# Optimization experiments

Measured on AMD Instinct MI355X. Metric: run time of the kernel, lower is better.

## Reference

```python
import jax, jax.numpy as jnp
import numpy as np

EPS = 1e-4  # matches init_kwargs eps


def setup_inputs() -> dict:
    key = jax.random.key(0)
    k1, k2, k3 = jax.random.split(key, 3)
    B, C, T = 64, 256, 2048
    x = jax.random.normal(k1, (B, C, T), dtype=jnp.float32)
    # per-timestep BatchNorm affine params: [T, C]
    gamma = 1.0 + 0.1 * jax.random.normal(k2, (T, C), dtype=jnp.float32)
    beta = 0.01 * jax.random.normal(k3, (T, C), dtype=jnp.float32)
    return {"x": x, "gamma": gamma, "beta": beta}


def reference(x, gamma, beta):
    # BNTTv1 (training mode): every timestep's BatchNorm1d sees the FULL [B, C, T]
    # tensor, so the batch statistics (per-channel mean/var over B and T) are
    # identical across timesteps. Only the affine (gamma_t, beta_t) differs, and
    # the module keeps just slice t of layer t's output. Equivalent fused form:
    mean = jnp.mean(x, axis=(0, 2), keepdims=True)            # [1, C, 1]
    var = jnp.mean((x - mean) ** 2, axis=(0, 2), keepdims=True)  # biased var
    norm = (x - mean) * jax.lax.rsqrt(var + EPS)              # [B, C, T]
    # gamma/beta: [T, C] -> broadcast as [1, C, T]
    out = norm * gamma.T[None, :, :] + beta.T[None, :, :]
    return out
```

## Files before the change

### kernel.cpp

```cpp
#include <hip/hip_runtime.h>

#define B_ 64
#define C_ 256
#define T_ 2048
#define EPS_ 1e-4f
#define NPC ((float)(B_ * T_))

#define T4 (T_ / 4)
#define CG_ 8

#define CTILE 16
#define T4TILE 16
#define BCHUNK 32

typedef float f4 __attribute__((ext_vector_type(4)));

__global__ __launch_bounds__(256) void bntt_stats(const float* __restrict__ x,
                                                  float* __restrict__ partials) {
    const int bid = blockIdx.x;
    const int b   = bid >> 5;
    const int cg  = bid & 31;
    const int tid = threadIdx.x;
    const f4* p = (const f4*)(x + ((size_t)b * C_ + (size_t)cg * CG_) * T_);

    float sum[CG_], ssq[CG_];
    #pragma unroll
    for (int k = 0; k < CG_; ++k) { sum[k] = 0.0f; ssq[k] = 0.0f; }

    #pragma unroll
    for (int i = 0; i < 16; ++i) {
        f4 v = p[tid + i * 256];
        const int k = i >> 1;
        sum[k] += v.x + v.y + v.z + v.w;
        ssq[k] += v.x * v.x + v.y * v.y + v.z * v.z + v.w * v.w;
    }

    __shared__ float ls[CG_][256];
    __shared__ float lq[CG_][256];
    #pragma unroll
    for (int k = 0; k < CG_; ++k) { ls[k][tid] = sum[k]; lq[k][tid] = ssq[k]; }
    __syncthreads();

    const int k = tid >> 5;
    const int j = tid & 31;
    float S = 0.0f, SS = 0.0f;
    #pragma unroll
    for (int m = 0; m < 8; ++m) {
        S  += ls[k][j + m * 32];
        SS += lq[k][j + m * 32];
    }
    #pragma unroll
    for (int off = 16; off > 0; off >>= 1) {
        S  += __shfl_down(S, off);
        SS += __shfl_down(SS, off);
    }
    if (j == 0) {
        const size_t c = (size_t)cg * CG_ + k;
        partials[(size_t)b * C_ + c]                      = S;
        partials[(size_t)B_ * C_ + (size_t)b * C_ + c]    = SS;
    }
}

__global__ __launch_bounds__(256) void bntt_norm(const float* __restrict__ x,
                                                 const float* __restrict__ gamma,
                                                 const float* __restrict__ beta,
                                                 const float* __restrict__ partials,
                                                 float* __restrict__ out) {
    __shared__ float sg[64][17];
    __shared__ float sb[64][17];
    __shared__ float psum[CTILE][8], psq[CTILE][8];
    __shared__ float smean[CTILE], sistd[CTILE];

    const int tid    = threadIdx.x;
    const int tile   = blockIdx.x & 511;
    const int c0     = (tile >> 5) * CTILE;
    const int t4base = (tile & 31) * T4TILE;
    const int b0     = (blockIdx.x >> 9) * BCHUNK;

    {
        const int cl  = tid & 15;
        const int tl0 = tid >> 4;
        const int tbase = t4base * 4;
        #pragma unroll
        for (int it = 0; it < 4; ++it) {
            const int tl = tl0 + it * 16;
            const size_t gi = (size_t)(tbase + tl) * C_ + (c0 + cl);
            sg[tl][cl] = gamma[gi];
            sb[tl][cl] = beta[gi];
        }
    }

    if (tid < 128) {
        const int cl = tid & 15;
        const int h  = tid >> 4;
        const int c  = c0 + cl;
        float S = 0.0f, SS = 0.0f;
        #pragma unroll
        for (int m = 0; m < 8; ++m) {
            const size_t b = (size_t)(h * 8 + m);
            S  += partials[b * C_ + c];
            SS += partials[(size_t)B_ * C_ + b * C_ + c];
        }
        psum[cl][h] = S;
        psq[cl][h]  = SS;
    }
    __syncthreads();

    if (tid < CTILE) {
        float S = 0.0f, SS = 0.0f;
        #pragma unroll
        for (int h = 0; h < 8; ++h) { S += psum[tid][h]; SS += psq[tid][h]; }
        const float mean = S / NPC;
        smean[tid] = mean;
        sistd[tid] = rsqrtf(SS / NPC - mean * mean + EPS_);
    }
    __syncthreads();

    const int t4i = tid & 15;
    const int ci  = tid >> 4;
    const float mean = smean[ci];
    const float istd = sistd[ci];
    f4 sc, sh;
    #pragma unroll
    for (int j = 0; j < 4; ++j) {
        const int tl = t4i * 4 + j;
        const float s1 = sg[tl][ci] * istd;
        ((float*)&sc)[j] = s1;
        ((float*)&sh)[j] = fmaf(-mean, s1, sb[tl][ci]);
    }

    size_t idx = ((size_t)b0 * C_ + (c0 + ci)) * T4 + (t4base + t4i);
    const size_t step = (size_t)C_ * T4;
    #pragma unroll 8
    for (int b = 0; b < BCHUNK; ++b) {
        f4 xv = ((const f4*)x)[idx];
        f4 o;
        o.x = fmaf(xv.x, sc.x, sh.x);
        o.y = fmaf(xv.y, sc.y, sh.y);
        o.z = fmaf(xv.z, sc.z, sh.z);
        o.w = fmaf(xv.w, sc.w, sh.w);
        __builtin_nontemporal_store(o, &((f4*)out)[idx]);
        idx += step;
    }
}

#define SPLITS 8
#define BPB (B_ / SPLITS)
__global__ __launch_bounds__(256) void bntt_stats_fb(const float* __restrict__ x,
                                                     float* __restrict__ partials) {
    const int c   = blockIdx.x & (C_ - 1);
    const int s   = blockIdx.x >> 8;
    const int tid = threadIdx.x;
    float sum = 0.0f, sumsq = 0.0f;
    const int b0 = s * BPB;
    #pragma unroll
    for (int b = 0; b < BPB; ++b) {
        const f4* p = (const f4*)(x + (size_t)(b0 + b) * (C_ * T_) + (size_t)c * T_);
        #pragma unroll
        for (int i = 0; i < T4 / 256; ++i) {
            f4 v = p[tid + i * 256];
            sum   += v.x + v.y + v.z + v.w;
            sumsq += v.x * v.x + v.y * v.y + v.z * v.z + v.w * v.w;
        }
    }
    #pragma unroll
    for (int off = 32; off > 0; off >>= 1) {
        sum   += __shfl_down(sum, off);
        sumsq += __shfl_down(sumsq, off);
    }
    __shared__ float ls2[4], lss2[4];
    const int wave = tid >> 6, lane = tid & 63;
    if (lane == 0) { ls2[wave] = sum; lss2[wave] = sumsq; }
    __syncthreads();
    if (tid == 0) {
        partials[s * C_ + c]               = ls2[0] + ls2[1] + ls2[2] + ls2[3];
        partials[SPLITS * C_ + s * C_ + c] = lss2[0] + lss2[1] + lss2[2] + lss2[3];
    }
}

__global__ __launch_bounds__(256) void bntt_norm_fb(const float* __restrict__ x,
                                                    const float* __restrict__ gamma,
                                                    const float* __restrict__ beta,
                                                    const float* __restrict__ partials,
                                                    float* __restrict__ out) {
    const int p   = (blockIdx.x & 511) * 256 + threadIdx.x;
    const int c   = p >> 9;
    const int t4  = p & (T4 - 1);
    const int t   = t4 * 4;
    const int b0  = (blockIdx.x >> 9) * BCHUNK;

    float S = 0.0f, SS = 0.0f;
    #pragma unroll
    for (int s = 0; s < SPLITS; ++s) {
        S  += partials[s * C_ + c];
        SS += partials[SPLITS * C_ + s * C_ + c];
    }
    const float mean = S / NPC;
    const float istd = rsqrtf(SS / NPC - mean * mean + EPS_);

    f4 sc, sh;
    #pragma unroll
    for (int j = 0; j < 4; ++j) {
        float g  = gamma[(size_t)(t + j) * C_ + c];
        float bb = beta [(size_t)(t + j) * C_ + c];
        float s1 = g * istd;
        ((float*)&sc)[j] = s1;
        ((float*)&sh)[j] = fmaf(-mean, s1, bb);
    }
    size_t idx = (size_t)(b0 * C_ + c) * T4 + t4;
    const size_t step = (size_t)C_ * T4;
    #pragma unroll 8
    for (int b = 0; b < BCHUNK; ++b) {
        f4 xv = ((const f4*)x)[idx];
        f4 o;
        o.x = fmaf(xv.x, sc.x, sh.x);
        o.y = fmaf(xv.y, sc.y, sh.y);
        o.z = fmaf(xv.z, sc.z, sh.z);
        o.w = fmaf(xv.w, sc.w, sh.w);
        __builtin_nontemporal_store(o, &((f4*)out)[idx]);
        idx += step;
    }
}

extern "C" void kernel_launch(void* const* d_in, const int* in_sizes, int n_in,
                              void* d_out, int out_size, void* d_ws, size_t ws_size,
                              hipStream_t stream) {
    const float* x     = (const float*)d_in[0];
    const float* gamma = (const float*)d_in[1];
    const float* beta  = (const float*)d_in[2];
    float* out = (float*)d_out;
    float* partials = (float*)d_ws;

    const int ngrid = (C_ / CTILE) * (T4 / T4TILE) * (B_ / BCHUNK);

    if (ws_size >= (size_t)2 * B_ * C_ * sizeof(float)) {
        bntt_stats<<<B_ * (C_ / CG_), 256, 0, stream>>>(x, partials);
        bntt_norm<<<ngrid, 256, 0, stream>>>(x, gamma, beta, partials, out);
    } else {
        bntt_stats_fb<<<C_ * SPLITS, 256, 0, stream>>>(x, partials);
        bntt_norm_fb<<<ngrid, 256, 0, stream>>>(x, gamma, beta, partials, out);
    }
}
```

Baseline: 256.4 us.

## Fuse stats and normalize into one persistent kernel with global atomic barrier

```diff
diff --git a/kernel.cpp b/kernel.cpp
--- a/kernel.cpp
+++ b/kernel.cpp
@@ -9,74 +9,82 @@
 #define T4 (T_ / 4)
 #define CG_ 8
 
+#define NBLK 1024
 #define CTILE 16
 #define T4TILE 16
 #define BCHUNK 32
 
 typedef float f4 __attribute__((ext_vector_type(4)));
 
-__global__ __launch_bounds__(256) void bntt_stats(const float* __restrict__ x,
-                                                  float* __restrict__ partials) {
+__global__ __launch_bounds__(256, 6) void bntt_onepass(const float* __restrict__ x,
+                                                       const float* __restrict__ gamma,
+                                                       const float* __restrict__ beta,
+                                                       float* __restrict__ out,
+                                                       float* __restrict__ ws) {
+    float* partials   = ws;
+    unsigned int* bar = (unsigned int*)(ws + 2 * B_ * C_);
+
+    const int tid = threadIdx.x;
     const int bid = blockIdx.x;
-    const int b   = bid >> 5;
-    const int cg  = bid & 31;
-    const int tid = threadIdx.x;
-    const f4* p = (const f4*)(x + ((size_t)b * C_ + (size_t)cg * CG_) * T_);
-
-    float sum[CG_], ssq[CG_];
-    #pragma unroll
-    for (int k = 0; k < CG_; ++k) { sum[k] = 0.0f; ssq[k] = 0.0f; }
-
-    #pragma unroll
-    for (int i = 0; i < 16; ++i) {
-        f4 v = p[tid + i * 256];
-        const int k = i >> 1;
-        sum[k] += v.x + v.y + v.z + v.w;
-        ssq[k] += v.x * v.x + v.y * v.y + v.z * v.z + v.w * v.w;
-    }
 
     __shared__ float ls[CG_][256];
     __shared__ float lq[CG_][256];
-    #pragma unroll
-    for (int k = 0; k < CG_; ++k) { ls[k][tid] = sum[k]; lq[k][tid] = ssq[k]; }
-    __syncthreads();
-
-    const int k = tid >> 5;
-    const int j = tid & 31;
-    float S = 0.0f, SS = 0.0f;
-    #pragma unroll
-    for (int m = 0; m < 8; ++m) {
-        S  += ls[k][j + m * 32];
-        SS += lq[k][j + m * 32];
-    }
-    #pragma unroll
-    for (int off = 16; off > 0; off >>= 1) {
-        S  += __shfl_down(S, off);
-        SS += __shfl_down(SS, off);
-    }
-    if (j == 0) {
-        const size_t c = (size_t)cg * CG_ + k;
-        partials[(size_t)b * C_ + c]                      = S;
-        partials[(size_t)B_ * C_ + (size_t)b * C_ + c]    = SS;
-    }
-}
-
-__global__ __launch_bounds__(256) void bntt_norm(const float* __restrict__ x,
-                                                 const float* __restrict__ gamma,
-                                                 const float* __restrict__ beta,
-                                                 const float* __restrict__ partials,
-                                                 float* __restrict__ out) {
-    __shared__ float sg[64][17];
-    __shared__ float sb[64][17];
     __shared__ float psum[CTILE][8], psq[CTILE][8];
     __shared__ float smean[CTILE], sistd[CTILE];
 
-    const int tid    = threadIdx.x;
-    const int tile   = blockIdx.x & 511;
+    const int ab    = bid >> 4;
+    const int cpair = bid & 15;
+    #pragma unroll
+    for (int half = 0; half < 2; ++half) {
+        const int cbase = cpair * (2 * CG_) + half * CG_;
+        const f4* p = (const f4*)(x + ((size_t)ab * C_ + cbase) * T_);
+
+        float sum[CG_], ssq[CG_];
+        #pragma unroll
+        for (int k = 0; k < CG_; ++k) { sum[k] = 0.0f; ssq[k] = 0.0f; }
+        #pragma unroll
+        for (int i = 0; i < 16; ++i) {
+            f4 v = p[tid + i * 256];
+            const int k = i >> 1;
+            sum[k] += v.x + v.y + v.z + v.w;
+            ssq[k] += v.x * v.x + v.y * v.y + v.z * v.z + v.w * v.w;
+        }
+        #pragma unroll
+        for (int k = 0; k < CG_; ++k) { ls[k][tid] = sum[k]; lq[k][tid] = ssq[k]; }
+        __syncthreads();
+
+        const int k = tid >> 5;
+        const int j = tid & 31;
+        float S = 0.0f, SS = 0.0f;
+        #pragma unroll
+        for (int m = 0; m < 8; ++m) {
+            S  += ls[k][j + m * 32];
+            SS += lq[k][j + m * 32];
+        }
+        #pragma unroll
+        for (int off = 16; off > 0; off >>= 1) {
+            S  += __shfl_down(S, off);
+            SS += __shfl_down(SS, off);
+        }
+        if (j == 0) {
+            const size_t c = (size_t)cbase + k;
+            __hip_atomic_store(&partials[(size_t)ab * C_ + c], S,
+                               __ATOMIC_RELAXED, __HIP_MEMORY_SCOPE_AGENT);
+            __hip_atomic_store(&partials[(size_t)B_ * C_ + (size_t)ab * C_ + c], SS,
+                               __ATOMIC_RELAXED, __HIP_MEMORY_SCOPE_AGENT);
+        }
+        __syncthreads();
+    }
+    if (tid == 0)
+        __hip_atomic_fetch_add(bar, 1u, __ATOMIC_RELEASE, __HIP_MEMORY_SCOPE_AGENT);
+
+    const int tile   = bid & 511;
     const int c0     = (tile >> 5) * CTILE;
     const int t4base = (tile & 31) * T4TILE;
-    const int b0     = (blockIdx.x >> 9) * BCHUNK;
-
+    const int b0     = (bid >> 9) * BCHUNK;
+
+    float (*sg)[17] = (float (*)[17])ls;
+    float (*sb)[17] = (float (*)[17])lq;
     {
         const int cl  = tid & 15;
         const int tl0 = tid >> 4;
@@ -90,22 +98,30 @@
         }
     }
 
+    if (tid == 0) {
+        while (__hip_atomic_load(bar, __ATOMIC_ACQUIRE, __HIP_MEMORY_SCOPE_AGENT)
+               < (unsigned int)NBLK)
+            __builtin_amdgcn_s_sleep(2);
+    }
+    __syncthreads();
+
     if (tid < 128) {
         const int cl = tid & 15;
         const int h  = tid >> 4;
-        const int c  = c0 + cl;
+        const size_t c = (size_t)(c0 + cl);
         float S = 0.0f, SS = 0.0f;
         #pragma unroll
         for (int m = 0; m < 8; ++m) {
-            const size_t b = (size_t)(h * 8 + m);
-            S  += partials[b * C_ + c];
-            SS += partials[(size_t)B_ * C_ + b * C_ + c];
+            const size_t bb = (size_t)(h * 8 + m);
+            S  += __hip_atomic_load(&partials[bb * C_ + c],
+                                    __ATOMIC_RELAXED, __HIP_MEMORY_SCOPE_AGENT);
+            SS += __hip_atomic_load(&partials[(size_t)B_ * C_ + bb * C_ + c],
+                                    __ATOMIC_RELAXED, __HIP_MEMORY_SCOPE_AGENT);
         }
         psum[cl][h] = S;
         psq[cl][h]  = SS;
     }
     __syncthreads();
-
     if (tid < CTILE) {
         float S = 0.0f, SS = 0.0f;
         #pragma unroll
@@ -229,15 +245,16 @@
     const float* gamma = (const float*)d_in[1];
     const float* beta  = (const float*)d_in[2];
     float* out = (float*)d_out;
-    float* partials = (float*)d_ws;
-
-    const int ngrid = (C_ / CTILE) * (T4 / T4TILE) * (B_ / BCHUNK);
-
-    if (ws_size >= (size_t)2 * B_ * C_ * sizeof(float)) {
-        bntt_stats<<<B_ * (C_ / CG_), 256, 0, stream>>>(x, partials);
-        bntt_norm<<<ngrid, 256, 0, stream>>>(x, gamma, beta, partials, out);
+    float* wsf = (float*)d_ws;
+
+    const size_t need = (size_t)2 * B_ * C_ * sizeof(float) + sizeof(unsigned int);
+
+    if (ws_size >= need) {
+        hipMemsetAsync((void*)(wsf + 2 * B_ * C_), 0, sizeof(unsigned int), stream);
+        bntt_onepass<<<NBLK, 256, 0, stream>>>(x, gamma, beta, out, wsf);
     } else {
-        bntt_stats_fb<<<C_ * SPLITS, 256, 0, stream>>>(x, partials);
-        bntt_norm_fb<<<ngrid, 256, 0, stream>>>(x, gamma, beta, partials, out);
-    }
-}
+        bntt_stats_fb<<<C_ * SPLITS, 256, 0, stream>>>(x, wsf);
+        const int ngrid = (C_ / CTILE) * (T4 / T4TILE) * (B_ / BCHUNK);
+        bntt_norm_fb<<<ngrid, 256, 0, stream>>>(x, gamma, beta, wsf, out);
+    }
+}
```

New measurement: 369.9 us. 44.3% more time.
